# Kernel tuning notes

Measured on AMD Instinct MI355X. Metric: run time of the kernel, lower is better.

The kernel has to match this reference:

```python
import jax, jax.numpy as jnp
import numpy as np

D_MODEL = 1024
N_HEADS = 16
D_HEAD = D_MODEL // N_HEADS


def setup_inputs() -> dict:
    key = jax.random.key(0)
    k1, k2, k3 = jax.random.split(key, 3)
    x = jax.random.normal(k1, (4, 2048, D_MODEL), dtype=jnp.float32)
    # nn.Linear weights stored [out, in]; we keep that convention.
    s = 1.0 / np.sqrt(D_MODEL)
    W_qkv = jax.random.uniform(k2, (3 * D_MODEL, D_MODEL), dtype=jnp.float32, minval=-s, maxval=s)
    W_out = jax.random.uniform(k3, (D_MODEL, D_MODEL), dtype=jnp.float32, minval=-s, maxval=s)
    return {"x": x, "W_qkv": W_qkv, "W_out": W_out}


def reference(x, W_qkv, W_out):
    B, T, C = x.shape
    qkv = jnp.einsum('btc,oc->bto', x, W_qkv)  # [B,T,3C]
    q, k, v = jnp.split(qkv, 3, axis=-1)

    def split_heads(t):
        return t.reshape(B, T, N_HEADS, D_HEAD).transpose(0, 2, 1, 3)  # [B,H,T,Dh]

    q, k, v = split_heads(q), split_heads(k), split_heads(v)
    scale = D_HEAD ** -0.5
    scores = jnp.einsum('bhqd,bhkd->bhqk', q, k) * scale  # [B,H,T,T]
    mask = jnp.triu(jnp.ones((T, T), dtype=bool), k=1)
    scores = jnp.where(mask, -jnp.inf, scores)
    att = jax.nn.softmax(scores, axis=-1)
    out = jnp.einsum('bhqk,bhkd->bhqd', att, v)
    out = out.transpose(0, 2, 1, 3).reshape(B, T, C)
    return jnp.einsum('btc,oc->bto', out, W_out)
```

## Files before the change

kernel.cpp:

```cpp
#include <hip/hip_runtime.h>
#include <hip/hip_bf16.h>
#include <math.h>


typedef __attribute__((ext_vector_type(8))) short bf16x8;
typedef __attribute__((ext_vector_type(4))) float f32x4;

__device__ __forceinline__ void async16(const void* g, void* l) {
    __builtin_amdgcn_global_load_lds((const __attribute__((address_space(1))) void*)g,
                                     (__attribute__((address_space(3))) void*)l,
                                     16, 0, 0);
}

__device__ __forceinline__ unsigned short f2b(float f) {
    __hip_bfloat16 h = __float2bfloat16(f);
    return *(unsigned short*)&h;
}

__device__ __forceinline__ unsigned int packbf2(float a, float b) {
    __hip_bfloat162 h2 = __float22bfloat162_rn(make_float2(a, b));
    return *(unsigned int*)&h2;
}

__global__ __launch_bounds__(256)
void cast3_f32_bf16(const float* __restrict__ a, unsigned short* __restrict__ oa, int na,
                    const float* __restrict__ b, unsigned short* __restrict__ ob, int nb,
                    const float* __restrict__ c, unsigned short* __restrict__ oc, int nc)
{
    const int bid  = blockIdx.x;
    const int na_b = na >> 11;
    const int nb_b = nb >> 11;
    const float* in;
    unsigned short* out;
    int base;
    if (bid < na_b)             { in = a; out = oa; base = bid; }
    else if (bid < na_b + nb_b) { in = b; out = ob; base = bid - na_b; }
    else                        { in = c; out = oc; base = bid - na_b - nb_b; }
    int i = (base * 256 + threadIdx.x) * 8;
    float4 x = *(const float4*)(in + i);
    float4 y = *(const float4*)(in + i + 4);
    __hip_bfloat16 r[8];
    r[0] = __float2bfloat16(x.x); r[1] = __float2bfloat16(x.y);
    r[2] = __float2bfloat16(x.z); r[3] = __float2bfloat16(x.w);
    r[4] = __float2bfloat16(y.x); r[5] = __float2bfloat16(y.y);
    r[6] = __float2bfloat16(y.z); r[7] = __float2bfloat16(y.w);
    *(float4*)(out + i) = *(float4*)r;
}

#define BAR8 __builtin_amdgcn_s_barrier()
#define LGKM0_PIN do { asm volatile("s_waitcnt lgkmcnt(0)" ::: "memory"); \
                       __builtin_amdgcn_sched_barrier(0); } while (0)
#define VMCNT_PIN(n) do { asm volatile("s_waitcnt vmcnt(" #n ")" ::: "memory"); \
                          __builtin_amdgcn_sched_barrier(0); } while (0)

#define LOAD_A_ALL(B_) do { \
    _Pragma("unroll") \
    for (int mi = 0; mi < 8; ++mi) { \
        af[mi][0] = *(const bf16x8*)&smem[(B_)*16384 + baseA0 + mi*1024]; \
        af[mi][1] = *(const bf16x8*)&smem[(B_)*16384 + baseA1 + mi*1024]; \
    } } while (0)

#define LOAD_B2(B_, QN) do { \
    _Pragma("unroll") \
    for (int ni = 0; ni < 2; ++ni) { \
        bf[ni][0] = *(const bf16x8*)&smem[(B_)*16384 + baseB0 + ((QN)*2+ni)*1024]; \
        bf[ni][1] = *(const bf16x8*)&smem[(B_)*16384 + baseB1 + ((QN)*2+ni)*1024]; \
    } } while (0)

#define MFMA16(QM, QN) do { \
    _Pragma("unroll") \
    for (int mi = 0; mi < 4; ++mi) { \
        _Pragma("unroll") \
        for (int ni = 0; ni < 2; ++ni) { \
            acc[(QM)*4+mi][(QN)*2+ni] = __builtin_amdgcn_mfma_f32_16x16x32_bf16( \
                af[(QM)*4+mi][0], bf[ni][0], acc[(QM)*4+mi][(QN)*2+ni], 0, 0, 0); \
            acc[(QM)*4+mi][(QN)*2+ni] = __builtin_amdgcn_mfma_f32_16x16x32_bf16( \
                af[(QM)*4+mi][1], bf[ni][1], acc[(QM)*4+mi][(QN)*2+ni], 0, 0, 0); \
        } } } while (0)

#define STAGE_A8(B_, H_, T_) do { \
    const unsigned short* g_ = A + (size_t)(m0 + (H_)*128) * K + (T_)*64; \
    async16(g_ + g0, &smem[(B_)*16384 + (H_)*8192 + lds0]); \
    async16(g_ + g1, &smem[(B_)*16384 + (H_)*8192 + lds1]); } while (0)

#define STAGE_B8(B_, H_, T_) do { \
    const unsigned short* g_ = Bt + (size_t)(n0 + (H_)*128) * K + (T_)*64; \
    async16(g_ + g0, &smem[32768 + (B_)*16384 + (H_)*8192 + lds0]); \
    async16(g_ + g1, &smem[32768 + (B_)*16384 + (H_)*8192 + lds1]); } while (0)

__global__ __launch_bounds__(512, 2)
void gemm_bf16_nt_8ph(const unsigned short* __restrict__ A,
                      const unsigned short* __restrict__ Bt,
                      unsigned short* __restrict__ C,
                      int M, int N, int K, int sc_ncols, float sc)
{
    __shared__ unsigned short smem[65536];

    const int tid  = threadIdx.x;
    const int lane = tid & 63;
    const int wave = tid >> 6;
    const int wm   = wave >> 2;
    const int wn   = wave & 3;
    const int fr   = lane & 15;
    const int q    = lane >> 4;

    const int ntn = N >> 8;
    int wg = blockIdx.x;
    const int nwg = gridDim.x;
    if ((nwg & 7) == 0) {
        const int cpx = nwg >> 3;
        wg = (wg & 7) * cpx + (wg >> 3);
    }
    const int m0 = (wg / ntn) << 8;
    const int n0 = (wg % ntn) << 8;

    const int c0 = tid, c1 = 512 + tid;
    const int r0 = c0 >> 3, r1 = c1 >> 3;
    const int g0 = r0 * K + (((c0 & 7) ^ (r0 & 7)) << 3);
    const int g1 = r1 * K + (((c1 & 7) ^ (r1 & 7)) << 3);
    const int lds0 = wave * 512;
    const int lds1 = 4096 + wave * 512;

    const int baseA0 = (wm*128 + fr) * 64 + (((0) | q) ^ (fr & 7)) * 8;
    const int baseA1 = (wm*128 + fr) * 64 + (((4) | q) ^ (fr & 7)) * 8;
    const int baseB0 = 32768 + (wn*64 + fr) * 64 + (((0) | q) ^ (fr & 7)) * 8;
    const int baseB1 = 32768 + (wn*64 + fr) * 64 + (((4) | q) ^ (fr & 7)) * 8;

    f32x4 acc[8][4];
#pragma unroll
    for (int i = 0; i < 8; ++i)
#pragma unroll
        for (int j = 0; j < 4; ++j) acc[i][j] = (f32x4){0.f, 0.f, 0.f, 0.f};

    bf16x8 af[8][2];
    bf16x8 bf[2][2];

    STAGE_A8(0, 0, 0); STAGE_A8(0, 1, 0); STAGE_B8(0, 0, 0); STAGE_B8(0, 1, 0);
    STAGE_A8(1, 0, 1); STAGE_A8(1, 1, 1); STAGE_B8(1, 0, 1);
    VMCNT_PIN(6);
    BAR8;

    const int niter = K >> 7;
#pragma unroll 1
    for (int i = 0; i < niter; ++i) {
        const int t1 = 2*i + 1, t2 = 2*i + 2, t3 = 2*i + 3;
        const bool st = (i < niter - 1);

        LOAD_A_ALL(0); LOAD_B2(0, 0);
        STAGE_B8(1, 1, t1);
        BAR8; LGKM0_PIN;
        __builtin_amdgcn_s_setprio(1); MFMA16(0, 0); __builtin_amdgcn_s_setprio(0);
        BAR8;
        if (st) STAGE_A8(0, 0, t2);
        BAR8; LGKM0_PIN;
        __builtin_amdgcn_s_setprio(1); MFMA16(1, 0); __builtin_amdgcn_s_setprio(0);
        BAR8;
        LOAD_B2(0, 1);
        if (st) STAGE_A8(0, 1, t2);
        BAR8; LGKM0_PIN;
        __builtin_amdgcn_s_setprio(1); MFMA16(0, 1); __builtin_amdgcn_s_setprio(0);
        BAR8;
        if (st) STAGE_B8(0, 0, t2);
        BAR8; LGKM0_PIN;
        __builtin_amdgcn_s_setprio(1); MFMA16(1, 1); __builtin_amdgcn_s_setprio(0);
        if (st) { VMCNT_PIN(6); } else { VMCNT_PIN(0); }
        BAR8;
        LOAD_A_ALL(1); LOAD_B2(1, 0);
        if (st) STAGE_B8(0, 1, t2);
        BAR8; LGKM0_PIN;
        __builtin_amdgcn_s_setprio(1); MFMA16(0, 0); __builtin_amdgcn_s_setprio(0);
        BAR8;
        if (st) STAGE_A8(1, 0, t3);
        BAR8; LGKM0_PIN;
        __builtin_amdgcn_s_setprio(1); MFMA16(1, 0); __builtin_amdgcn_s_setprio(0);
        BAR8;
        LOAD_B2(1, 1);
        if (st) STAGE_A8(1, 1, t3);
        BAR8; LGKM0_PIN;
        __builtin_amdgcn_s_setprio(1); MFMA16(0, 1); __builtin_amdgcn_s_setprio(0);
        BAR8;
        if (st) STAGE_B8(1, 0, t3);
        BAR8; LGKM0_PIN;
        __builtin_amdgcn_s_setprio(1); MFMA16(1, 1); __builtin_amdgcn_s_setprio(0);
        if (st) VMCNT_PIN(6);
        BAR8;
    }

    const int ccol  = n0 + wn * 64 + fr;
    const int crow0 = m0 + wm * 128 + q * 4;
#pragma unroll
    for (int mi = 0; mi < 8; ++mi) {
#pragma unroll
        for (int r = 0; r < 4; ++r) {
            const size_t row = (size_t)(crow0 + mi * 16 + r);
#pragma unroll
            for (int ni = 0; ni < 4; ++ni) {
                float mult = (ccol + ni * 16 < sc_ncols) ? sc : 1.0f;
                C[row * N + ccol + ni * 16] = f2b(acc[mi][ni][r] * mult);
            }
        }
    }
}

template <typename OutT>
__global__ __launch_bounds__(256)
void gemm_bf16_nt(const unsigned short* __restrict__ A,
                  const unsigned short* __restrict__ Bt,
                  OutT* __restrict__ C, int M, int N, int K,
                  int sc_ncols, float sc)
{
    __shared__ unsigned short As[2 * 128 * 32];
    __shared__ unsigned short Bs[2 * 128 * 32];
    const int tid  = threadIdx.x;
    const int lane = tid & 63;
    const int wave = tid >> 6;
    const int wm   = wave >> 1;
    const int wn   = wave & 1;
    const int m0   = blockIdx.y * 128;
    const int n0   = blockIdx.x * 128;

    f32x4 acc[4][4];
#pragma unroll
    for (int i = 0; i < 4; ++i)
#pragma unroll
        for (int j = 0; j < 4; ++j) acc[i][j] = (f32x4){0.f, 0.f, 0.f, 0.f};

    const int srow = tid >> 2;
    const int scol = (tid & 3) * 8;
    const int wbase = wave * 512;
    const int fr = lane & 15;
    const int fk = (lane >> 4) * 8;

    for (int k0 = 0; k0 < K; k0 += 64) {
#pragma unroll
        for (int ks = 0; ks < 2; ++ks) {
#pragma unroll
            for (int c = 0; c < 2; ++c) {
                const unsigned short* ga =
                    A + (size_t)(m0 + c * 64 + srow) * K + k0 + ks * 32 + scol;
                async16(ga, As + ks * 4096 + c * 2048 + wbase);
                const unsigned short* gb =
                    Bt + (size_t)(n0 + c * 64 + srow) * K + k0 + ks * 32 + scol;
                async16(gb, Bs + ks * 4096 + c * 2048 + wbase);
            }
        }
        __syncthreads();

#pragma unroll
        for (int ks = 0; ks < 2; ++ks) {
            bf16x8 af[4], bfr[4];
#pragma unroll
            for (int mi = 0; mi < 4; ++mi)
                af[mi] = *(const bf16x8*)&As[ks * 4096 + (wm * 64 + mi * 16 + fr) * 32 + fk];
#pragma unroll
            for (int ni = 0; ni < 4; ++ni)
                bfr[ni] = *(const bf16x8*)&Bs[ks * 4096 + (wn * 64 + ni * 16 + fr) * 32 + fk];
#pragma unroll
            for (int mi = 0; mi < 4; ++mi)
#pragma unroll
                for (int ni = 0; ni < 4; ++ni)
                    acc[mi][ni] = __builtin_amdgcn_mfma_f32_16x16x32_bf16(
                        af[mi], bfr[ni], acc[mi][ni], 0, 0, 0);
        }
        __syncthreads();
    }

    const int ccol  = n0 + wn * 64 + (lane & 15);
    const int crow0 = m0 + wm * 64 + (lane >> 4) * 4;
#pragma unroll
    for (int mi = 0; mi < 4; ++mi) {
#pragma unroll
        for (int r = 0; r < 4; ++r) {
            const size_t row = (size_t)(crow0 + mi * 16 + r);
#pragma unroll
            for (int ni = 0; ni < 4; ++ni) {
                float mult = (ccol + ni * 16 < sc_ncols) ? sc : 1.0f;
                float v = acc[mi][ni][r] * mult;
                if constexpr (__is_same(OutT, float)) {
                    C[row * N + ccol + ni * 16] = v;
                } else {
                    C[row * N + ccol + ni * 16] = f2b(v);
                }
            }
        }
    }
}

__global__ __launch_bounds__(256)
void transpose_v(const unsigned short* __restrict__ qkv, unsigned short* __restrict__ vt, int T)
{
    __shared__ unsigned short tile[64 * 72];
    const int tid = threadIdx.x;
    const int k0  = blockIdx.x * 64;
    const int h   = blockIdx.y;
    const int b   = blockIdx.z;
    const size_t C3 = 3072;
    const unsigned short* vb = qkv + (size_t)b * T * C3 + 2048 + h * 64;

    const int r  = tid >> 2;
    const int c0 = (tid & 3) * 16;
    {
        const unsigned short* g = vb + (size_t)(k0 + r) * C3 + c0;
        *(float4*)&tile[r * 72 + c0]     = *(const float4*)g;
        *(float4*)&tile[r * 72 + c0 + 8] = *(const float4*)(g + 8);
    }
    __syncthreads();
    unsigned short buf[16];
#pragma unroll
    for (int j = 0; j < 16; ++j) buf[j] = tile[(c0 + j) * 72 + r];
    unsigned short* o = vt + ((size_t)(b * 16 + h) * 64 + r) * T + k0 + c0;
    *(float4*)o       = *(float4*)&buf[0];
    *(float4*)(o + 8) = *(float4*)&buf[8];
}

__global__ __launch_bounds__(256, 4)
void attn_mfma(const unsigned short* __restrict__ qkv,
               const unsigned short* __restrict__ vt,
               unsigned short* __restrict__ out, int T)
{
    __shared__ unsigned short Ks[64 * 72];
    __shared__ unsigned short Vts[64 * 72];
    __shared__ unsigned short Ps[2][64 * 72];

    const int tid  = threadIdx.x;
    const int lane = tid & 63;
    const int wave = tid >> 6;
    const int lc   = lane & 15;
    const int quad = lane >> 4;
    const int nq   = T >> 6;
    const int bid  = blockIdx.x;
    const int bh   = bid & 63;
    const int a    = bid >> 6;
    const int b    = bh >> 4;
    const int h    = bh & 15;
    int qt[2];
    qt[0] = nq - 1 - a;
    qt[1] = a;
    const size_t C3 = 3072;
    const unsigned short* qb  = qkv + (size_t)b * T * C3 + h * 64;
    const unsigned short* kb  = qb + 1024;
    const unsigned short* vtb = vt + (size_t)(b * 16 + h) * 64 * T;

    const int sr = tid >> 2;
    const int sc = (tid & 3) * 16;

    const int qrow = wave * 16 + lc;
    bf16x8 qf[2][2];
#pragma unroll
    for (int t = 0; t < 2; ++t) {
        const unsigned short* gq = qb + (size_t)(qt[t] * 64 + qrow) * C3 + quad * 8;
        qf[t][0] = *(const bf16x8*)gq;
        qf[t][1] = *(const bf16x8*)(gq + 32);
    }

    f32x4 o_[2][4];
    float l_[2];
#pragma unroll
    for (int t = 0; t < 2; ++t) {
        l_[t] = 0.f;
#pragma unroll
        for (int i = 0; i < 4; ++i) o_[t][i] = (f32x4){0.f, 0.f, 0.f, 0.f};
    }

    const float MB = 8.0f;

    for (int kt = 0; kt <= qt[0]; ++kt) {
        const int k0 = kt * 64;
        const unsigned short* gk = kb + (size_t)(k0 + sr) * C3 + sc;
        float4 kv0 = *(const float4*)gk;
        float4 kv1 = *(const float4*)(gk + 8);
        const unsigned short* gv = vtb + (size_t)sr * T + k0 + sc;
        float4 vv0 = *(const float4*)gv;
        float4 vv1 = *(const float4*)(gv + 8);

        __syncthreads();
        *(float4*)&Ks[sr * 72 + sc]      = kv0;
        *(float4*)&Ks[sr * 72 + sc + 8]  = kv1;
        *(float4*)&Vts[sr * 72 + sc]     = vv0;
        *(float4*)&Vts[sr * 72 + sc + 8] = vv1;
        __syncthreads();

        bf16x8 ak[4][2];
#pragma unroll
        for (int mi = 0; mi < 4; ++mi) {
            ak[mi][0] = *(const bf16x8*)&Ks[(mi * 16 + lc) * 72 + quad * 8];
            ak[mi][1] = *(const bf16x8*)&Ks[(mi * 16 + lc) * 72 + 32 + quad * 8];
        }

#pragma unroll
        for (int t = 0; t < 2; ++t) {
            if (t == 1 && kt > qt[1]) break;
            f32x4 s[4];
#pragma unroll
            for (int mi = 0; mi < 4; ++mi) {
                s[mi] = (f32x4){0.f, 0.f, 0.f, 0.f};
                s[mi] = __builtin_amdgcn_mfma_f32_16x16x32_bf16(ak[mi][0], qf[t][0], s[mi], 0, 0, 0);
                s[mi] = __builtin_amdgcn_mfma_f32_16x16x32_bf16(ak[mi][1], qf[t][1], s[mi], 0, 0, 0);
            }
            if (kt == qt[t]) {
                const int qg = qt[t] * 64 + wave * 16 + lc;
                const int kbase = k0 + quad * 4;
#pragma unroll
                for (int mi = 0; mi < 4; ++mi)
#pragma unroll
                    for (int r = 0; r < 4; ++r)
                        if (kbase + mi * 16 + r > qg)
                            s[mi][r] = -__builtin_inff();
            }
            float lacc = 0.f;
            const int prow = (wave * 16 + lc) * 72 + quad * 4;
#pragma unroll
            for (int mi = 0; mi < 4; ++mi) {
                float p0 = __builtin_amdgcn_exp2f(s[mi][0] - MB);
                float p1 = __builtin_amdgcn_exp2f(s[mi][1] - MB);
                float p2 = __builtin_amdgcn_exp2f(s[mi][2] - MB);
                float p3 = __builtin_amdgcn_exp2f(s[mi][3] - MB);
                lacc += (p0 + p1) + (p2 + p3);
                uint2 pk;
                pk.x = packbf2(p0, p1);
                pk.y = packbf2(p2, p3);
                *(uint2*)&Ps[t][prow + mi * 16] = pk;
            }
            l_[t] += lacc;
        }

        bf16x8 av[4][2];
#pragma unroll
        for (int mi = 0; mi < 4; ++mi) {
            av[mi][0] = *(const bf16x8*)&Vts[(mi * 16 + lc) * 72 + quad * 8];
            av[mi][1] = *(const bf16x8*)&Vts[(mi * 16 + lc) * 72 + 32 + quad * 8];
        }

#pragma unroll
        for (int t = 0; t < 2; ++t) {
            if (t == 1 && kt > qt[1]) break;
            bf16x8 bp0 = *(const bf16x8*)&Ps[t][(wave * 16 + lc) * 72 + quad * 8];
            bf16x8 bp1 = *(const bf16x8*)&Ps[t][(wave * 16 + lc) * 72 + 32 + quad * 8];
#pragma unroll
            for (int mi = 0; mi < 4; ++mi) {
                o_[t][mi] = __builtin_amdgcn_mfma_f32_16x16x32_bf16(av[mi][0], bp0, o_[t][mi], 0, 0, 0);
                o_[t][mi] = __builtin_amdgcn_mfma_f32_16x16x32_bf16(av[mi][1], bp1, o_[t][mi], 0, 0, 0);
            }
        }
    }

#pragma unroll
    for (int t = 0; t < 2; ++t) {
        float rs = l_[t];
        rs += __shfl_xor(rs, 16);
        rs += __shfl_xor(rs, 32);
        float inv = 1.f / rs;
        unsigned short* ob = out + ((size_t)b * T + qt[t] * 64 + wave * 16 + lc) * 1024
                           + h * 64 + quad * 4;
#pragma unroll
        for (int mi = 0; mi < 4; ++mi) {
            uint2 pk;
            pk.x = packbf2(o_[t][mi][0] * inv, o_[t][mi][1] * inv);
            pk.y = packbf2(o_[t][mi][2] * inv, o_[t][mi][3] * inv);
            *(uint2*)(ob + mi * 16) = pk;
        }
    }
}

extern "C" void kernel_launch(void* const* d_in, const int* in_sizes, int n_in,
                              void* d_out, int out_size, void* d_ws, size_t ws_size,
                              hipStream_t stream)
{
    const float* x     = (const float*)d_in[0];
    const float* W_qkv = (const float*)d_in[1];
    const float* W_out = (const float*)d_in[2];
    float* out = (float*)d_out;

    const int C = 1024;
    const int T = 2048;
    const int M = in_sizes[0] / C;
    const int B = M / T;
    const int n_x    = in_sizes[0];
    const int n_wqkv = in_sizes[1];
    const int n_wout = in_sizes[2];

    unsigned short* x_bf    = (unsigned short*)d_ws;
    unsigned short* wqkv_bf = x_bf    + n_x;
    unsigned short* wout_bf = wqkv_bf + n_wqkv;
    unsigned short* qkv_bf  = wout_bf + n_wout;
    unsigned short* vt_bf   = qkv_bf  + (size_t)M * 3 * C;
    unsigned short* ao_bf   = vt_bf   + (size_t)B * 16 * 64 * T;

    cast3_f32_bf16<<<(n_x + n_wqkv + n_wout) / 2048, 256, 0, stream>>>(
        x, x_bf, n_x, W_qkv, wqkv_bf, n_wqkv, W_out, wout_bf, n_wout);

    const float QSC = 0.18033688011112042f;
    gemm_bf16_nt_8ph<<<dim3(((3*C) / 256) * (M / 256)), 512, 0, stream>>>(
        x_bf, wqkv_bf, qkv_bf, M, 3*C, C, C, QSC);

    transpose_v<<<dim3(T/64, 16, B), 256, 0, stream>>>(qkv_bf, vt_bf, T);

    const int nq = T / 64;
    attn_mfma<<<dim3(B * 16 * (nq / 2)), 256, 0, stream>>>(qkv_bf, vt_bf, ao_bf, T);

    gemm_bf16_nt<float><<<dim3(C/128, M/128), 256, 0, stream>>>(
        ao_bf, wout_bf, out, M, C, C, 0, 1.0f);
}
```

Baseline: 250.7 us.

## Split A-fragment LDS loads into halves and reschedule staging in GEMM main loop

The GEMM inner loop now loads the A fragments from LDS in two halves, each just before the MFMA block that uses it, instead of loading all eight fragments up front. Global-to-LDS staging is reordered so the B tiles for the next buffer are issued inside the loop rather than in the prologue, and the vmcnt waits change from 6 to 4 to match. The intent is to interleave LDS reads with MFMA work and shorten the latency exposed at the start of each half-iteration. The risk is in the wait counts: if the reordered staging and the new vmcnt/lgkmcnt values do not line up, the kernel can read LDS before it is filled, and the extra barriers may add stalls.

```diff
diff --git a/kernel.cpp b/kernel.cpp
--- a/kernel.cpp
+++ b/kernel.cpp
@@ -48,16 +48,16 @@
 }
 
 #define BAR8 __builtin_amdgcn_s_barrier()
-#define LGKM0_PIN do { asm volatile("s_waitcnt lgkmcnt(0)" ::: "memory"); \
-                       __builtin_amdgcn_sched_barrier(0); } while (0)
+#define LGKM_PIN(n) do { asm volatile("s_waitcnt lgkmcnt(" #n ")" ::: "memory"); \
+                         __builtin_amdgcn_sched_barrier(0); } while (0)
 #define VMCNT_PIN(n) do { asm volatile("s_waitcnt vmcnt(" #n ")" ::: "memory"); \
                           __builtin_amdgcn_sched_barrier(0); } while (0)
 
-#define LOAD_A_ALL(B_) do { \
+#define LOAD_A_HALF(B_, QM) do { \
     _Pragma("unroll") \
-    for (int mi = 0; mi < 8; ++mi) { \
-        af[mi][0] = *(const bf16x8*)&smem[(B_)*16384 + baseA0 + mi*1024]; \
-        af[mi][1] = *(const bf16x8*)&smem[(B_)*16384 + baseA1 + mi*1024]; \
+    for (int mi = 0; mi < 4; ++mi) { \
+        af[(QM)*4+mi][0] = *(const bf16x8*)&smem[(B_)*16384 + baseA0 + ((QM)*4+mi)*1024]; \
+        af[(QM)*4+mi][1] = *(const bf16x8*)&smem[(B_)*16384 + baseA1 + ((QM)*4+mi)*1024]; \
     } } while (0)
 
 #define LOAD_B2(B_, QN) do { \
@@ -136,8 +136,8 @@
     bf16x8 bf[2][2];
 
     STAGE_A8(0, 0, 0); STAGE_A8(0, 1, 0); STAGE_B8(0, 0, 0); STAGE_B8(0, 1, 0);
-    STAGE_A8(1, 0, 1); STAGE_A8(1, 1, 1); STAGE_B8(1, 0, 1);
-    VMCNT_PIN(6);
+    STAGE_A8(1, 0, 1); STAGE_A8(1, 1, 1);
+    VMCNT_PIN(4);
     BAR8;
 
     const int niter = K >> 7;
@@ -146,43 +146,47 @@
         const int t1 = 2*i + 1, t2 = 2*i + 2, t3 = 2*i + 3;
         const bool st = (i < niter - 1);
 
-        LOAD_A_ALL(0); LOAD_B2(0, 0);
+        LOAD_A_HALF(0, 0); LOAD_B2(0, 0);
+        STAGE_B8(1, 0, t1);
+        LGKM_PIN(8);
+        BAR8; LGKM_PIN(0);
+        __builtin_amdgcn_s_setprio(1); MFMA16(0, 0); __builtin_amdgcn_s_setprio(0);
+        BAR8;
+        LOAD_A_HALF(0, 1);
         STAGE_B8(1, 1, t1);
-        BAR8; LGKM0_PIN;
+        BAR8; LGKM_PIN(0);
+        __builtin_amdgcn_s_setprio(1); MFMA16(1, 0); __builtin_amdgcn_s_setprio(0);
+        BAR8;
+        LOAD_B2(0, 1);
+        if (st) STAGE_A8(0, 0, t2);
+        BAR8; LGKM_PIN(0);
+        __builtin_amdgcn_s_setprio(1); MFMA16(0, 1); __builtin_amdgcn_s_setprio(0);
+        BAR8;
+        if (st) STAGE_A8(0, 1, t2);
+        BAR8;
+        __builtin_amdgcn_s_setprio(1); MFMA16(1, 1); __builtin_amdgcn_s_setprio(0);
+        if (st) { VMCNT_PIN(4); } else { VMCNT_PIN(0); }
+        BAR8;
+        LOAD_A_HALF(1, 0); LOAD_B2(1, 0);
+        if (st) STAGE_B8(0, 0, t2);
+        LGKM_PIN(8);
+        BAR8; LGKM_PIN(0);
         __builtin_amdgcn_s_setprio(1); MFMA16(0, 0); __builtin_amdgcn_s_setprio(0);
         BAR8;
-        if (st) STAGE_A8(0, 0, t2);
-        BAR8; LGKM0_PIN;
+        LOAD_A_HALF(1, 1);
+        if (st) STAGE_B8(0, 1, t2);
+        BAR8; LGKM_PIN(0);
         __builtin_amdgcn_s_setprio(1); MFMA16(1, 0); __builtin_amdgcn_s_setprio(0);
         BAR8;
-        LOAD_B2(0, 1);
-        if (st) STAGE_A8(0, 1, t2);
-        BAR8; LGKM0_PIN;
+        LOAD_B2(1, 1);
+        if (st) STAGE_A8(1, 0, t3);
+        BAR8; LGKM_PIN(0);
         __builtin_amdgcn_s_setprio(1); MFMA16(0, 1); __builtin_amdgcn_s_setprio(0);
         BAR8;
-        if (st) STAGE_B8(0, 0, t2);
-        BAR8; LGKM0_PIN;
+        if (st) STAGE_A8(1, 1, t3);
+        BAR8;
         __builtin_amdgcn_s_setprio(1); MFMA16(1, 1); __builtin_amdgcn_s_setprio(0);
-        if (st) { VMCNT_PIN(6); } else { VMCNT_PIN(0); }
-        BAR8;
-        LOAD_A_ALL(1); LOAD_B2(1, 0);
-        if (st) STAGE_B8(0, 1, t2);
-        BAR8; LGKM0_PIN;
-        __builtin_amdgcn_s_setprio(1); MFMA16(0, 0); __builtin_amdgcn_s_setprio(0);
-        BAR8;
-        if (st) STAGE_A8(1, 0, t3);
-        BAR8; LGKM0_PIN;
-        __builtin_amdgcn_s_setprio(1); MFMA16(1, 0); __builtin_amdgcn_s_setprio(0);
-        BAR8;
-        LOAD_B2(1, 1);
-        if (st) STAGE_A8(1, 1, t3);
-        BAR8; LGKM0_PIN;
-        __builtin_amdgcn_s_setprio(1); MFMA16(0, 1); __builtin_amdgcn_s_setprio(0);
-        BAR8;
-        if (st) STAGE_B8(1, 0, t3);
-        BAR8; LGKM0_PIN;
-        __builtin_amdgcn_s_setprio(1); MFMA16(1, 1); __builtin_amdgcn_s_setprio(0);
-        if (st) VMCNT_PIN(6);
+        if (st) VMCNT_PIN(4);
         BAR8;
     }
 
```

Result: no change. 246.8 us (-1.6%).
